# Optimization experiments

Measured on AMD Instinct MI355X. Metric: run time of the kernel, lower is better.

Reference implementation:

```python
import jax, jax.numpy as jnp
import numpy as np

N = 8192
F_IN = 128
OC1 = 64
OC2 = 64
N_CLASS = 16
AVG_DEG = 32.0


def setup_inputs() -> dict:
    key = jax.random.key(0)
    ks = jax.random.split(key, 10)
    # sparse-ish 0/1 adjacency with guaranteed self-loops (every row nonempty)
    A = (jax.random.uniform(ks[0], (N, N)) < (AVG_DEG / N)).astype(jnp.float32)
    A = jnp.maximum(A, jnp.eye(N, dtype=jnp.float32))
    deg = jnp.sum(A, axis=1)                      # [N]
    D = jnp.diag(deg)                             # diagonal degree matrix [N,N]
    X = jax.random.normal(ks[1], (N, F_IN), dtype=jnp.float32)
    s = 0.05
    W1 = jax.random.normal(ks[2], (F_IN, OC1), dtype=jnp.float32) * s
    b1 = jax.random.normal(ks[3], (OC1,), dtype=jnp.float32) * s
    W2 = jax.random.normal(ks[4], (OC1, OC2), dtype=jnp.float32) * s
    b2 = jax.random.normal(ks[5], (OC2,), dtype=jnp.float32) * s
    W3 = jax.random.normal(ks[6], (OC2, N_CLASS), dtype=jnp.float32) * s
    b3 = jax.random.normal(ks[7], (N_CLASS,), dtype=jnp.float32) * s
    return {"D": D, "X": X, "A": A, "W1": W1, "b1": b1,
            "W2": W2, "b2": b2, "W3": W3, "b3": b3}


def reference(D, X, A, W1, b1, W2, b2, W3, b3):
    # per-node degree: max over each row of the diagonal degree matrix
    deg = jnp.max(D, axis=1)                      # [N]
    # dj[0] in the original = degree of the FIRST (lowest-index) neighbor of i
    first_idx = jnp.argmax(A > 0, axis=1)         # [N]
    deg_first = deg[first_idx]                    # [N]
    # w[i,j] = A[i,j] / sqrt(deg_first[i] * deg[j]); zero where A[i,j]==0
    W = A / jnp.sqrt(deg_first[:, None] * deg[None, :])  # [N,N]

    def conv(H, Wl, bl):
        agg = W @ H                               # normalized neighbor aggregation
        return jax.nn.leaky_relu(agg @ Wl + bl)   # Linear + LeakyReLU(0.01)

    H = conv(X, W1, b1)
    # F.dropout in eval mode = identity
    H = conv(H, W2, b2)
    logits = H @ W3 + b3                          # [N, class_num]
    return jax.nn.log_softmax(logits, axis=1)
```

## Files before the change

### kernel.cpp

```cpp
#include <hip/hip_runtime.h>

#define NN   8192
#define FIN  128
#define CAP  128

__global__ __launch_bounds__(256) void k_scan(
        const float* __restrict__ A,
        int* __restrict__ deg,
        int* __restrict__ first,
        int* __restrict__ cols,
        float* __restrict__ rsd) {
    __shared__ int s_cols[CAP];
    __shared__ int s_cnt, s_min;

    const int row = blockIdx.x;
    const int t   = threadIdx.x;
    if (t == 0) { s_cnt = 0; s_min = 0x7fffffff; }
    __syncthreads();

    const uint4* Arow = (const uint4*)(A + (size_t)row * NN);
    int lmin = 0x7fffffff;
#pragma unroll
    for (int v = 0; v < 8; ++v) {
        const int chunk = t + 256 * v;
        uint4 q = Arow[chunk];
        if (q.x | q.y | q.z | q.w) {
            unsigned int w[4] = {q.x, q.y, q.z, q.w};
#pragma unroll
            for (int h = 0; h < 4; ++h) {
                if (w[h]) {
                    int c = chunk * 4 + h;
                    int p = atomicAdd(&s_cnt, 1);
                    if (p < CAP) s_cols[p] = c;
                    lmin = min(lmin, c);
                }
            }
        }
    }
    if (lmin != 0x7fffffff) atomicMin(&s_min, lmin);
    __syncthreads();

    const int n = min(s_cnt, CAP);
    if (t < n) cols[row * CAP + t] = s_cols[t];
    if (t == 0) {
        deg[row]   = s_cnt;
        first[row] = s_min;
        rsd[row]   = 1.0f / sqrtf((float)s_cnt);
    }
}

__global__ __launch_bounds__(128) void k_agg1(
        const float* __restrict__ X,
        const float* __restrict__ rsd,
        const float* __restrict__ W1,
        const float* __restrict__ b1,
        const int* __restrict__ deg,
        const int* __restrict__ first,
        const int* __restrict__ cols,
        float* __restrict__ H1) {
    __shared__ int   s_cols[CAP];
    __shared__ float s_rsd[CAP];
    __shared__ float s_agg[FIN];

    const int row = blockIdx.x;
    const int t   = threadIdx.x;
    const int n   = min(deg[row], CAP);

    if (t < n) {
        int c = cols[row * CAP + t];
        s_cols[t] = c;
        s_rsd[t]  = rsd[c];
    }
    __syncthreads();

    {
        const float alpha = rsd[first[row]];
        float acc = 0.f;
        int k = 0;
        for (; k + 4 <= n; k += 4) {
            int c0 = s_cols[k], c1 = s_cols[k+1], c2 = s_cols[k+2], c3 = s_cols[k+3];
            float x0 = X[(size_t)c0 * FIN + t];
            float x1 = X[(size_t)c1 * FIN + t];
            float x2 = X[(size_t)c2 * FIN + t];
            float x3 = X[(size_t)c3 * FIN + t];
            acc += s_rsd[k] * x0 + s_rsd[k+1] * x1 + s_rsd[k+2] * x2 + s_rsd[k+3] * x3;
        }
        for (; k < n; ++k)
            acc += s_rsd[k] * X[(size_t)s_cols[k] * FIN + t];
        s_agg[t] = alpha * acc;
    }
    __syncthreads();

    if (t < 64) {
        float acc = b1[t];
#pragma unroll 8
        for (int f = 0; f < FIN; ++f)
            acc += s_agg[f] * W1[f * 64 + t];
        H1[(size_t)row * 64 + t] = acc > 0.f ? acc : 0.01f * acc;
    }
}

__global__ __launch_bounds__(64) void k_agg2(
        const float* __restrict__ H1,
        const float* __restrict__ rsd,
        const float* __restrict__ W2,
        const float* __restrict__ b2,
        const float* __restrict__ W3,
        const float* __restrict__ b3,
        const int* __restrict__ deg,
        const int* __restrict__ first,
        const int* __restrict__ cols,
        float* __restrict__ out) {
    __shared__ int   s_cols[CAP];
    __shared__ float s_rsd[CAP];
    __shared__ float s_agg[64];
    __shared__ float s_h2[64];
    __shared__ float s_logit[16];

    const int row = blockIdx.x;
    const int t   = threadIdx.x;
    const int n   = min(deg[row], CAP);

    for (int k = t; k < n; k += 64) {
        int c = cols[row * CAP + k];
        s_cols[k] = c;
        s_rsd[k]  = rsd[c];
    }
    __syncthreads();

    float acc = 0.f;
    {
        int k = 0;
        for (; k + 4 <= n; k += 4) {
            int c0 = s_cols[k], c1 = s_cols[k+1], c2 = s_cols[k+2], c3 = s_cols[k+3];
            float h0 = H1[(size_t)c0 * 64 + t];
            float h1 = H1[(size_t)c1 * 64 + t];
            float h2 = H1[(size_t)c2 * 64 + t];
            float h3 = H1[(size_t)c3 * 64 + t];
            acc += s_rsd[k] * h0 + s_rsd[k+1] * h1 + s_rsd[k+2] * h2 + s_rsd[k+3] * h3;
        }
        for (; k < n; ++k)
            acc += s_rsd[k] * H1[(size_t)s_cols[k] * 64 + t];
    }
    s_agg[t] = rsd[first[row]] * acc;
    __syncthreads();

    float a2 = b2[t];
#pragma unroll 8
    for (int f = 0; f < 64; ++f)
        a2 += s_agg[f] * W2[f * 64 + t];
    s_h2[t] = a2 > 0.f ? a2 : 0.01f * a2;
    __syncthreads();

    if (t < 16) {
        float lg = b3[t];
#pragma unroll 8
        for (int f = 0; f < 64; ++f)
            lg += s_h2[f] * W3[f * 16 + t];
        s_logit[t] = lg;
    }
    __syncthreads();

    if (t < 16) {
        float m = -1e30f;
#pragma unroll
        for (int k = 0; k < 16; ++k) m = fmaxf(m, s_logit[k]);
        float s = 0.f;
#pragma unroll
        for (int k = 0; k < 16; ++k) s += expf(s_logit[k] - m);
        out[row * 16 + t] = s_logit[t] - m - logf(s);
    }
}

extern "C" void kernel_launch(void* const* d_in, const int* in_sizes, int n_in,
                              void* d_out, int out_size, void* d_ws, size_t ws_size,
                              hipStream_t stream) {
    const float* X  = (const float*)d_in[1];
    const float* A  = (const float*)d_in[2];
    const float* W1 = (const float*)d_in[3];
    const float* b1 = (const float*)d_in[4];
    const float* W2 = (const float*)d_in[5];
    const float* b2 = (const float*)d_in[6];
    const float* W3 = (const float*)d_in[7];
    const float* b3 = (const float*)d_in[8];

    char* ws = (char*)d_ws;
    float* rsd   = (float*)(ws);
    int*   deg   = (int*)  (ws + 32768);
    int*   first = (int*)  (ws + 65536);
    float* H1    = (float*)(ws + 98304);
    int*   cols  = (int*)  (ws + 98304 + 2097152);

    k_scan<<<NN, 256, 0, stream>>>(A, deg, first, cols, rsd);
    k_agg1<<<NN, 128, 0, stream>>>(X, rsd, W1, b1, deg, first, cols, H1);
    k_agg2<<<NN,  64, 0, stream>>>(H1, rsd, W2, b2, W3, b3, deg, first, cols,
                                   (float*)d_out);
}
```

Before: 502.3 us.

## Use nontemporal A loads, 16-bit column indices, and float4 split-neighbor aggregation

The adjacency scan now reads A with nontemporal loads, and neighbor column indices are stored as 16-bit values to halve index traffic. Both aggregation kernels now split the neighbor list across thread groups that each gather float4 rows, and the partial sums are reduced in shared memory. The dense linear layers are split across twice as many threads, and the second kernel moves to 128 threads. This is meant to raise memory-level parallelism in the gathers and to avoid polluting the cache with the 256MB A stream, at the cost of extra syncs and shared-memory reductions.

```diff
diff --git a/kernel.cpp b/kernel.cpp
--- a/kernel.cpp
+++ b/kernel.cpp
@@ -3,12 +3,14 @@
 #define NN   8192
 #define FIN  128
 #define CAP  128
+
+typedef unsigned int u32x4 __attribute__((ext_vector_type(4)));
 
 __global__ __launch_bounds__(256) void k_scan(
         const float* __restrict__ A,
         int* __restrict__ deg,
         int* __restrict__ first,
-        int* __restrict__ cols,
+        unsigned short* __restrict__ cols,
         float* __restrict__ rsd) {
     __shared__ int s_cols[CAP];
     __shared__ int s_cnt, s_min;
@@ -18,12 +20,12 @@
     if (t == 0) { s_cnt = 0; s_min = 0x7fffffff; }
     __syncthreads();
 
-    const uint4* Arow = (const uint4*)(A + (size_t)row * NN);
+    const u32x4* Arow = (const u32x4*)(A + (size_t)row * NN);
     int lmin = 0x7fffffff;
 #pragma unroll
     for (int v = 0; v < 8; ++v) {
         const int chunk = t + 256 * v;
-        uint4 q = Arow[chunk];
+        u32x4 q = __builtin_nontemporal_load(Arow + chunk);
         if (q.x | q.y | q.z | q.w) {
             unsigned int w[4] = {q.x, q.y, q.z, q.w};
 #pragma unroll
@@ -41,7 +43,7 @@
     __syncthreads();
 
     const int n = min(s_cnt, CAP);
-    if (t < n) cols[row * CAP + t] = s_cols[t];
+    if (t < n) cols[row * CAP + t] = (unsigned short)s_cols[t];
     if (t == 0) {
         deg[row]   = s_cnt;
         first[row] = s_min;
@@ -56,11 +58,13 @@
         const float* __restrict__ b1,
         const int* __restrict__ deg,
         const int* __restrict__ first,
-        const int* __restrict__ cols,
+        const unsigned short* __restrict__ cols,
         float* __restrict__ H1) {
-    __shared__ int   s_cols[CAP];
+    __shared__ unsigned short s_cols[CAP];
     __shared__ float s_rsd[CAP];
+    __shared__ float s_part[4][FIN];
     __shared__ float s_agg[FIN];
+    __shared__ float s_lin[2][64];
 
     const int row = blockIdx.x;
     const int t   = threadIdx.x;
@@ -68,39 +72,45 @@
 
     if (t < n) {
         int c = cols[row * CAP + t];
-        s_cols[t] = c;
+        s_cols[t] = (unsigned short)c;
         s_rsd[t]  = rsd[c];
     }
     __syncthreads();
 
     {
-        const float alpha = rsd[first[row]];
-        float acc = 0.f;
-        int k = 0;
-        for (; k + 4 <= n; k += 4) {
-            int c0 = s_cols[k], c1 = s_cols[k+1], c2 = s_cols[k+2], c3 = s_cols[k+3];
-            float x0 = X[(size_t)c0 * FIN + t];
-            float x1 = X[(size_t)c1 * FIN + t];
-            float x2 = X[(size_t)c2 * FIN + t];
-            float x3 = X[(size_t)c3 * FIN + t];
-            acc += s_rsd[k] * x0 + s_rsd[k+1] * x1 + s_rsd[k+2] * x2 + s_rsd[k+3] * x3;
+        const int g = t >> 5, q = t & 31;
+        const float4* X4 = (const float4*)X;
+        float4 acc = make_float4(0.f, 0.f, 0.f, 0.f);
+        for (int k = g; k < n; k += 4) {
+            const float4 x = X4[(size_t)s_cols[k] * 32 + q];
+            const float  r = s_rsd[k];
+            acc.x += r * x.x; acc.y += r * x.y; acc.z += r * x.z; acc.w += r * x.w;
         }
-        for (; k < n; ++k)
-            acc += s_rsd[k] * X[(size_t)s_cols[k] * FIN + t];
-        s_agg[t] = alpha * acc;
-    }
-    __syncthreads();
-
-    if (t < 64) {
-        float acc = b1[t];
+        ((float4*)s_part[g])[q] = acc;
+    }
+    __syncthreads();
+
+    const float alpha = rsd[first[row]];
+    s_agg[t] = alpha * (s_part[0][t] + s_part[1][t] + s_part[2][t] + s_part[3][t]);
+    __syncthreads();
+
+    {
+        const int c = t & 63, h = t >> 6;
+        const int f0 = h * 64;
+        float acc = h ? 0.f : b1[c];
 #pragma unroll 8
-        for (int f = 0; f < FIN; ++f)
-            acc += s_agg[f] * W1[f * 64 + t];
-        H1[(size_t)row * 64 + t] = acc > 0.f ? acc : 0.01f * acc;
-    }
-}
-
-__global__ __launch_bounds__(64) void k_agg2(
+        for (int f = 0; f < 64; ++f)
+            acc += s_agg[f0 + f] * W1[(f0 + f) * 64 + c];
+        s_lin[h][c] = acc;
+    }
+    __syncthreads();
+    if (t < 64) {
+        float a = s_lin[0][t] + s_lin[1][t];
+        H1[(size_t)row * 64 + t] = a > 0.f ? a : 0.01f * a;
+    }
+}
+
+__global__ __launch_bounds__(128) void k_agg2(
         const float* __restrict__ H1,
         const float* __restrict__ rsd,
         const float* __restrict__ W2,
@@ -109,11 +119,13 @@
         const float* __restrict__ b3,
         const int* __restrict__ deg,
         const int* __restrict__ first,
-        const int* __restrict__ cols,
+        const unsigned short* __restrict__ cols,
         float* __restrict__ out) {
-    __shared__ int   s_cols[CAP];
+    __shared__ unsigned short s_cols[CAP];
     __shared__ float s_rsd[CAP];
+    __shared__ float s_part[8][64];
     __shared__ float s_agg[64];
+    __shared__ float s_lin[2][64];
     __shared__ float s_h2[64];
     __shared__ float s_logit[16];
 
@@ -121,44 +133,63 @@
     const int t   = threadIdx.x;
     const int n   = min(deg[row], CAP);
 
-    for (int k = t; k < n; k += 64) {
-        int c = cols[row * CAP + k];
-        s_cols[k] = c;
-        s_rsd[k]  = rsd[c];
-    }
-    __syncthreads();
-
-    float acc = 0.f;
-    {
-        int k = 0;
-        for (; k + 4 <= n; k += 4) {
-            int c0 = s_cols[k], c1 = s_cols[k+1], c2 = s_cols[k+2], c3 = s_cols[k+3];
-            float h0 = H1[(size_t)c0 * 64 + t];
-            float h1 = H1[(size_t)c1 * 64 + t];
-            float h2 = H1[(size_t)c2 * 64 + t];
-            float h3 = H1[(size_t)c3 * 64 + t];
-            acc += s_rsd[k] * h0 + s_rsd[k+1] * h1 + s_rsd[k+2] * h2 + s_rsd[k+3] * h3;
+    if (t < n) {
+        int c = cols[row * CAP + t];
+        s_cols[t] = (unsigned short)c;
+        s_rsd[t]  = rsd[c];
+    }
+    __syncthreads();
+
+    {
+        const int g = t >> 4, q = t & 15;
+        const float4* H4 = (const float4*)H1;
+        float4 acc = make_float4(0.f, 0.f, 0.f, 0.f);
+        for (int k = g; k < n; k += 8) {
+            const float4 x = H4[(size_t)s_cols[k] * 16 + q];
+            const float  r = s_rsd[k];
+            acc.x += r * x.x; acc.y += r * x.y; acc.z += r * x.z; acc.w += r * x.w;
         }
-        for (; k < n; ++k)
-            acc += s_rsd[k] * H1[(size_t)s_cols[k] * 64 + t];
-    }
-    s_agg[t] = rsd[first[row]] * acc;
-    __syncthreads();
-
-    float a2 = b2[t];
-#pragma unroll 8
-    for (int f = 0; f < 64; ++f)
-        a2 += s_agg[f] * W2[f * 64 + t];
-    s_h2[t] = a2 > 0.f ? a2 : 0.01f * a2;
-    __syncthreads();
-
-    if (t < 16) {
-        float lg = b3[t];
-#pragma unroll 8
-        for (int f = 0; f < 64; ++f)
-            lg += s_h2[f] * W3[f * 16 + t];
-        s_logit[t] = lg;
-    }
+        ((float4*)s_part[g])[q] = acc;
+    }
+    __syncthreads();
+
+    const float alpha = rsd[first[row]];
+    if (t < 64) {
+        float s = 0.f;
+#pragma unroll
+        for (int g = 0; g < 8; ++g) s += s_part[g][t];
+        s_agg[t] = alpha * s;
+    }
+    __syncthreads();
+
+    {
+        const int c = t & 63, h = t >> 6;
+        const int f0 = h * 32;
+        float acc = h ? 0.f : b2[c];
+#pragma unroll
+        for (int f = 0; f < 32; ++f)
+            acc += s_agg[f0 + f] * W2[(f0 + f) * 64 + c];
+        s_lin[h][c] = acc;
+    }
+    __syncthreads();
+    if (t < 64) {
+        float a = s_lin[0][t] + s_lin[1][t];
+        s_h2[t] = a > 0.f ? a : 0.01f * a;
+    }
+    __syncthreads();
+
+    if (t < 64) {
+        const int c = t & 15, h = t >> 4;
+        const int f0 = h * 16;
+        float acc = h ? 0.f : b3[c];
+#pragma unroll
+        for (int f = 0; f < 16; ++f)
+            acc += s_h2[f0 + f] * W3[(f0 + f) * 16 + c];
+        s_part[h][c] = acc;
+    }
+    __syncthreads();
+    if (t < 16)
+        s_logit[t] = s_part[0][t] + s_part[1][t] + s_part[2][t] + s_part[3][t];
     __syncthreads();
 
     if (t < 16) {
@@ -185,14 +216,14 @@
     const float* b3 = (const float*)d_in[8];
 
     char* ws = (char*)d_ws;
-    float* rsd   = (float*)(ws);
-    int*   deg   = (int*)  (ws + 32768);
-    int*   first = (int*)  (ws + 65536);
-    float* H1    = (float*)(ws + 98304);
-    int*   cols  = (int*)  (ws + 98304 + 2097152);
+    float*          rsd   = (float*)(ws);
+    int*            deg   = (int*)  (ws + 32768);
+    int*            first = (int*)  (ws + 65536);
+    float*          H1    = (float*)(ws + 98304);
+    unsigned short* cols  = (unsigned short*)(ws + 98304 + 2097152);
 
     k_scan<<<NN, 256, 0, stream>>>(A, deg, first, cols, rsd);
     k_agg1<<<NN, 128, 0, stream>>>(X, rsd, W1, b1, deg, first, cols, H1);
-    k_agg2<<<NN,  64, 0, stream>>>(H1, rsd, W2, b2, W3, b3, deg, first, cols,
+    k_agg2<<<NN, 128, 0, stream>>>(H1, rsd, W2, b2, W3, b3, deg, first, cols,
                                    (float*)d_out);
 }
```

New measurement: 479.8 us. 4.5% less time.
